# Optimization experiments

Hardware: AMD Instinct MI355X
Metric: run time of the kernel (lower is better)

Reference implementation:

```python
import jax, jax.numpy as jnp
import numpy as np

L = 256            # model length (match states)
Q = 2 * L + 3      # num_states = 2*length + 3
M = 1              # num_models
B = 256            # batch of sequences
T = 512            # sequence length (timesteps)
EPS = 1e-16


def setup_inputs() -> dict:
    key = jax.random.key(0)
    k1, k2, k3 = jax.random.split(key, 3)
    return {
        "emission_probs": jax.random.uniform(k1, (T, M, B, Q), dtype=jnp.float32),
        "log_A": jax.random.normal(k2, (M, Q, Q), dtype=jnp.float32),
        "init_logits": jax.random.normal(k3, (M, Q), dtype=jnp.float32),
    }


def reference(emission_probs, log_A, init_logits):
    # Dense transition matrix per model (row-stochastic), as in transitioner.make_log_A()
    A = jax.nn.softmax(log_A, axis=-1)                 # (M, Q, Q)
    init_dist = jax.nn.softmax(init_logits, axis=-1)   # (M, Q)

    def norm_step(E, R, ll):
        # One scaled-forward update: multiply emission, normalize, accumulate loglik.
        E = jnp.maximum(E, EPS)
        R = jnp.maximum(R, EPS)
        a = E * R                                      # (M, B, Q)
        S = jnp.sum(a, axis=-1, keepdims=True)         # (M, B, 1)
        ll = ll + jnp.log(S)
        a = a / S
        return a, ll

    # t = 0: init=True -> R is the initial distribution (no transition applied)
    R0 = jnp.broadcast_to(init_dist[:, None, :], (M, B, Q))
    fwd0, ll0 = norm_step(emission_probs[0], R0, jnp.zeros((M, B, 1), jnp.float32))
    out0 = jnp.concatenate([jnp.log(fwd0), ll0], axis=-1)  # (M, B, Q+1)

    def step(carry, E_t):
        fwd, ll = carry
        # transitioner(old_scaled_forward): dense transition matvec per model
        R = jnp.einsum('mbq,mqk->mbk', fwd, A)
        a, ll = norm_step(E_t, R, ll)
        return (a, ll), jnp.concatenate([jnp.log(a), ll], axis=-1)

    _, outs = jax.lax.scan(step, (fwd0, ll0), emission_probs[1:])
    outs = jnp.concatenate([out0[None], outs], axis=0)     # (T, M, B, Q+1)
    # RNN output layout: (M*B, T, Q+1)
    return jnp.transpose(outs, (1, 2, 0, 3)).reshape(M * B, T, Q + 1)
```

## Files before the change

### kernel.cpp

```cpp
#include <hip/hip_runtime.h>
#include <cstdint>

#define Qn   515
#define QP   520
#define QP2  528
#define Bn   256
#define Tn   512
#define OQ   516
#define EPSc 1e-16f
#define NSL  65
#define NT   5
#define KT   33
#define KTA  17
#define USTR 532
#define NGRP 32
#define NBLK 8

#define WS_AMAT 0
#define WS_INIT (544*520*4)
#define WS_UBUF (WS_INIT + 5120)
#define WS_PSUM (WS_UBUF + 2*NGRP*8*QP2*4)
#define WS_FLAG (WS_PSUM + 2*NGRP*8*8*4)
#define WS_TOTAL (WS_FLAG + NGRP*NBLK*64)

#define L_FRAG 0
#define L_UST  (NT*KT*64*8)
#define L_USL  (L_UST + 16*USTR*2)
#define L_SIG  (L_USL + 8*68*4)
#define LDS_TOTAL (L_SIG + 128)

typedef float f32x4 __attribute__((ext_vector_type(4)));
typedef short s16x4 __attribute__((ext_vector_type(4)));

__device__ __forceinline__ unsigned bfbits(float x) {
    unsigned u = __builtin_bit_cast(unsigned, x);
    unsigned r = u + 0x7FFFu + ((u >> 16) & 1u);
    return r >> 16;
}

__global__ void prep_A(const float* __restrict__ logA, float* __restrict__ AMAT) {
    __shared__ float red[4];
    __shared__ float srow[Qn];
    int row = blockIdx.x, tid = threadIdx.x;
    if (row >= Qn) {
        for (int c = tid; c < QP; c += 256) AMAT[(size_t)row*QP + c] = 0.f;
        return;
    }
    float mx = -1e30f;
    for (int c = tid; c < Qn; c += 256) { float x = logA[(size_t)row*Qn + c]; srow[c] = x; mx = fmaxf(mx, x); }
#pragma unroll
    for (int o = 32; o > 0; o >>= 1) mx = fmaxf(mx, __shfl_xor(mx, o));
    if ((tid & 63) == 0) red[tid >> 6] = mx;
    __syncthreads();
    mx = fmaxf(fmaxf(red[0], red[1]), fmaxf(red[2], red[3]));
    __syncthreads();
    float sm = 0.f;
    for (int c = tid; c < Qn; c += 256) sm += __expf(srow[c] - mx);
#pragma unroll
    for (int o = 32; o > 0; o >>= 1) sm += __shfl_xor(sm, o);
    if ((tid & 63) == 0) red[tid >> 6] = sm;
    __syncthreads();
    float inv = 1.f / (red[0] + red[1] + red[2] + red[3]);
    for (int c = tid; c < QP; c += 256)
        AMAT[(size_t)row*QP + c] = (c < Qn) ? __expf(srow[c] - mx) * inv : 0.f;
}

__global__ void prep_init(const float* __restrict__ il, float* __restrict__ INITD) {
    __shared__ float red[4];
    __shared__ float srow[Qn];
    int tid = threadIdx.x;
    float mx = -1e30f;
    for (int c = tid; c < Qn; c += 256) { float x = il[c]; srow[c] = x; mx = fmaxf(mx, x); }
#pragma unroll
    for (int o = 32; o > 0; o >>= 1) mx = fmaxf(mx, __shfl_xor(mx, o));
    if ((tid & 63) == 0) red[tid >> 6] = mx;
    __syncthreads();
    mx = fmaxf(fmaxf(red[0], red[1]), fmaxf(red[2], red[3]));
    __syncthreads();
    float sm = 0.f;
    for (int c = tid; c < Qn; c += 256) sm += __expf(srow[c] - mx);
#pragma unroll
    for (int o = 32; o > 0; o >>= 1) sm += __shfl_xor(sm, o);
    if ((tid & 63) == 0) red[tid >> 6] = sm;
    __syncthreads();
    float inv = 1.f / (red[0] + red[1] + red[2] + red[3]);
    for (int c = tid; c < QP; c += 256)
        INITD[c] = (c < Qn) ? __expf(srow[c] - mx) * inv : 0.f;
}

__global__ void __launch_bounds__(256, 1)
hmm_fwd(const float* __restrict__ E, const float* __restrict__ AMAT,
        const float* __restrict__ INITD, float* __restrict__ out,
        float* __restrict__ ubuf, float* __restrict__ psum,
        unsigned* __restrict__ flags)
{
    extern __shared__ char smem[];
    uint2*  frag   = (uint2*)(smem + L_FRAG);
    unsigned short* ustage = (unsigned short*)(smem + L_UST);
    float*  usl    = (float*)(smem + L_USL);
    float*  invs   = (float*)(smem + L_SIG);
    float*  lsig   = invs + 8;

    const int tid  = threadIdx.x;
    const int lane = tid & 63;
    const int wv   = tid >> 6;
    const int bid  = blockIdx.x;
    const int g    = bid & 31;
    const int j    = bid >> 5;
    const int b0   = g * 8;
    const int q0   = j * NSL;
    const int q0p  = j * 66;

    for (int f = tid; f < NT*KT*64; f += 256) {
        int tile = f >> 6, l = f & 63;
        int nt = tile / KT, kt = tile - nt*KT;
        int col = q0 + nt*16 + (l & 15);
        int kb  = kt*16 + ((l >> 4) << 2);
        float v[4];
#pragma unroll
        for (int i = 0; i < 4; ++i) {
            int pk_ = kb + i;
            int jr = pk_ / 66, rr = pk_ - jr*66;
            int qrow = (rr < 65) ? (jr*65 + rr) : -1;
            v[i] = (qrow >= 0 && col < QP) ? AMAT[(size_t)qrow*QP + col] : 0.f;
        }
        uint2 pk;
        pk.x = bfbits(v[0]) | (bfbits(v[1]) << 16);
        pk.y = bfbits(v[2]) | (bfbits(v[3]) << 16);
        frag[f] = pk;
    }
    for (int i = tid; i < 16*(USTR/2); i += 256) ((unsigned*)ustage)[i] = 0u;
    float llreg = 0.f;
    float ur0[9], ur1[9];
    __syncthreads();

    const int ntn = (wv == 0) ? 2 : 1;
    const int nts0 = wv;
    int eoff[2][4];
#pragma unroll
    for (int sl = 0; sl < 2; ++sl) {
#pragma unroll
        for (int r = 0; r < 4; ++r) {
            int nt  = sl ? 4 : nts0;
            int row = ((lane >> 4) << 2) + r;
            int col = nt*16 + (lane & 15);
            int q   = q0 + col;
            bool ok = (lane < 32) && (col < NSL) && (q < Qn) && (sl < ntn);
            eoff[sl][r] = ok ? ((b0 + row)*Qn + q) : -1;
        }
    }

    auto rowsum_store = [&](int wb, int snum) {
        int half = lane >> 5, c = lane & 31;
        int row = wv*2 + half;
        float v = usl[row*68 + c] + usl[row*68 + c + 32];
        if (c == 0) v += usl[row*68 + 64];
#pragma unroll
        for (int o = 16; o > 0; o >>= 1) v += __shfl_xor(v, o);
        if (c == 0)
            __hip_atomic_store(&psum[(((size_t)wb*NGRP + g)*8 + row)*8 + j], v,
                               __ATOMIC_RELAXED, __HIP_MEMORY_SCOPE_AGENT);
        float* ubr = ubuf + (((size_t)wb*NGRP + g)*8)*QP2 + q0p;
        for (int p = tid; p < 8*33; p += 256) {
            int rw = p/33, cl = p - rw*33;
            float a0 = usl[rw*68 + 2*cl];
            float a1 = (2*cl + 1 < NSL) ? usl[rw*68 + 2*cl + 1] : 0.f;
            uint64_t pk = (uint64_t)__builtin_bit_cast(unsigned, a0)
                        | ((uint64_t)__builtin_bit_cast(unsigned, a1) << 32);
            __hip_atomic_store((uint64_t*)(ubr + rw*QP2 + 2*cl), pk,
                               __ATOMIC_RELAXED, __HIP_MEMORY_SCOPE_AGENT);
        }
        __syncthreads();
        if (tid == 0)
            __hip_atomic_store(&flags[((unsigned)g*NBLK + j)*16], (unsigned)(snum + 1),
                               __ATOMIC_RELAXED, __HIP_MEMORY_SCOPE_AGENT);
    };

    auto spin_wait = [&](unsigned target) {
        if (tid < 8) {
            const unsigned* fp = flags + ((unsigned)g*NBLK + tid)*16;
            while (__hip_atomic_load(fp, __ATOMIC_RELAXED, __HIP_MEMORY_SCOPE_AGENT) < target)
                __builtin_amdgcn_s_sleep(1);
        }
        __syncthreads();
    };

    auto head_phase = [&](int rb, bool do_stage) {
        float ss = 0.f;
        if (tid < 8) {
            const float* pp = psum + (((size_t)rb*NGRP + g)*8 + tid)*8;
#pragma unroll
            for (int jj = 0; jj < 8; ++jj)
                ss += __hip_atomic_load(&pp[jj], __ATOMIC_RELAXED, __HIP_MEMORY_SCOPE_AGENT);
        }
        const float* ub = ubuf + (((size_t)rb*NGRP + g)*8)*QP2;
#pragma unroll
        for (int it = 0; it < 9; ++it) {
            int p = tid + it*256;
            bool ok = p < 8*264;
            int row = p / 264, kp = p - row*264;
            const uint64_t* ap = (const uint64_t*)(ub + (ok ? (row*QP2 + kp*2) : 0));
            uint64_t w = __hip_atomic_load(ap, __ATOMIC_RELAXED, __HIP_MEMORY_SCOPE_AGENT);
            ur0[it] = ok ? __builtin_bit_cast(float, (unsigned)(w & 0xffffffffu)) : 0.f;
            ur1[it] = ok ? __builtin_bit_cast(float, (unsigned)(w >> 32)) : 0.f;
        }
        if (tid < 8) {
            float ls = __logf(ss);
            invs[tid] = 1.f / ss;
            lsig[tid] = ls;
            llreg += ls;
        }
        __syncthreads();
        if (do_stage) {
#pragma unroll
            for (int it = 0; it < 9; ++it) {
                int p = tid + it*256;
                if (p < 8*264) {
                    int row = p / 264, kp = p - row*264;
                    float iv = invs[row];
                    ((unsigned*)ustage)[row*(USTR/2) + kp] =
                        bfbits(ur0[it]*iv) | (bfbits(ur1[it]*iv) << 16);
                }
            }
            __syncthreads();
        }
    };

    auto emit_outputs = [&](int tOut) {
        if (tid < 8 && j == 0)
            out[((size_t)(b0 + tid)*Tn + tOut)*OQ + Qn] = llreg;
#pragma unroll
        for (int it = 0; it < 9; ++it) {
            int p = tid + it*256;
            if (p < 8*264) {
                int row = p / 264, kp = p - row*264;
                int rr = kp*2 - q0p;
                if (rr >= 0 && rr < NSL) {
                    float ls = lsig[row];
                    int q = q0 + rr;
                    if (q < Qn)
                        out[((size_t)(b0+row)*Tn + tOut)*OQ + q]     = __logf(ur0[it]) - ls;
                    if (rr + 1 < NSL && q + 1 < Qn)
                        out[((size_t)(b0+row)*Tn + tOut)*OQ + q + 1] = __logf(ur1[it]) - ls;
                }
            }
        }
    };

    {
        for (int p = tid; p < 8*NSL; p += 256) {
            int row = p / NSL, col = p - row*NSL;
            int q = q0 + col;
            float uv = 0.f;
            if (q < Qn) {
                float e  = fmaxf(E[(size_t)(b0+row)*Qn + q], EPSc);
                float r0 = fmaxf(INITD[q], EPSc);
                uv = e * r0;
            }
            usl[row*68 + col] = uv;
        }
        __syncthreads();
        rowsum_store(0, 0);
    }

    for (int s = 1; s < Tn; ++s) {
        float ev[2][4];
        size_t ebase = (size_t)s * Bn * Qn;
#pragma unroll
        for (int sl = 0; sl < 2; ++sl)
#pragma unroll
            for (int r = 0; r < 4; ++r)
                ev[sl][r] = (eoff[sl][r] >= 0) ? E[ebase + eoff[sl][r]] : 0.f;

        spin_wait((unsigned)s);
        head_phase((s-1) & 1, true);

        f32x4 a0a = {0.f,0.f,0.f,0.f}, a0b = {0.f,0.f,0.f,0.f};
        f32x4 a1a = {0.f,0.f,0.f,0.f}, a1b = {0.f,0.f,0.f,0.f};
        {
            const unsigned short* urow = ustage + (lane & 15)*USTR + ((lane >> 4) << 2);
            const uint2* f0 = frag + (size_t)(nts0*KT)*64 + lane;
            const uint2* f1 = frag + (size_t)(4*KT)*64 + lane;
#pragma unroll 2
            for (int kt = 0; kt < KTA; ++kt) {
                s16x4 af = __builtin_bit_cast(s16x4, *(const uint2*)(urow + kt*16));
                a0a = __builtin_amdgcn_mfma_f32_16x16x16bf16_1k(af, __builtin_bit_cast(s16x4, f0[kt*64]), a0a, 0, 0, 0);
                if (ntn == 2)
                    a1a = __builtin_amdgcn_mfma_f32_16x16x16bf16_1k(af, __builtin_bit_cast(s16x4, f1[kt*64]), a1a, 0, 0, 0);
                int k2 = kt + KTA;
                if (k2 < KT) {
                    s16x4 af2 = __builtin_bit_cast(s16x4, *(const uint2*)(urow + k2*16));
                    a0b = __builtin_amdgcn_mfma_f32_16x16x16bf16_1k(af2, __builtin_bit_cast(s16x4, f0[k2*64]), a0b, 0, 0, 0);
                    if (ntn == 2)
                        a1b = __builtin_amdgcn_mfma_f32_16x16x16bf16_1k(af2, __builtin_bit_cast(s16x4, f1[k2*64]), a1b, 0, 0, 0);
                }
            }
        }
        if (lane < 32) {
#pragma unroll
            for (int r = 0; r < 4; ++r) {
                int row = ((lane >> 4) << 2) + r;
                {
                    int col = nts0*16 + (lane & 15);
                    if (col < NSL) {
                        float R = fmaxf(a0a[r] + a0b[r], EPSc);
                        int q = q0 + col;
                        usl[row*68 + col] = (q < Qn) ? fmaxf(ev[0][r], EPSc) * R : 0.f;
                    }
                }
                if (ntn == 2) {
                    int col = 64 + (lane & 15);
                    if (col < NSL) {
                        float R = fmaxf(a1a[r] + a1b[r], EPSc);
                        int q = q0 + col;
                        usl[row*68 + col] = (q < Qn) ? fmaxf(ev[1][r], EPSc) * R : 0.f;
                    }
                }
            }
        }
        __syncthreads();
        rowsum_store(s & 1, s);

        emit_outputs(s - 1);
    }

    spin_wait((unsigned)Tn);
    head_phase((Tn-1) & 1, false);
    emit_outputs(Tn - 1);
}

extern "C" void kernel_launch(void* const* d_in, const int* in_sizes, int n_in,
                              void* d_out, int out_size, void* d_ws, size_t ws_size,
                              hipStream_t stream) {
    (void)in_sizes; (void)n_in; (void)out_size;
    if (ws_size < (size_t)WS_TOTAL) return;

    const float* E    = (const float*)d_in[0];
    const float* logA = (const float*)d_in[1];
    const float* il   = (const float*)d_in[2];
    float* out = (float*)d_out;
    char*  ws  = (char*)d_ws;

    float*    AMAT  = (float*)(ws + WS_AMAT);
    float*    INITD = (float*)(ws + WS_INIT);
    float*    ubuf  = (float*)(ws + WS_UBUF);
    float*    psum  = (float*)(ws + WS_PSUM);
    unsigned* flags = (unsigned*)(ws + WS_FLAG);

    hipMemsetAsync(ws + WS_UBUF, 0, WS_TOTAL - WS_UBUF, stream);

    prep_A<<<544, 256, 0, stream>>>(logA, AMAT);
    prep_init<<<1, 256, 0, stream>>>(il, INITD);

    static_assert(LDS_TOTAL < 160*1024, "LDS budget");
    hipFuncSetAttribute(reinterpret_cast<const void*>(hmm_fwd),
                        hipFuncAttributeMaxDynamicSharedMemorySize, LDS_TOTAL);
    hmm_fwd<<<256, 256, LDS_TOTAL, stream>>>(E, AMAT, INITD, out, ubuf, psum, flags);
}
```

Measured before the change: 3.292 ms.

## Replace flag-based inter-block exchange with sequence-tagged values and workgroup-scope polling

Removes separate flags and partial-sum buffers. Each forward value is now packed with its timestep tag in a 64-bit word, and consumers poll the data words directly until all tags match. Each row's normalizer is computed redundantly from the full vector, so the per-block rowsum pass and a barrier go away. A startup probe checks whether blocks in a group can see each other through workgroup-scope (L1) loads with buffer_inv. If not, the kernel falls back to agent-scope dual stores. The transition matrix is also pre-packed to bf16 in the prep kernel. This relies on non-portable coherence assumptions and adds timing-dependent mode selection.

```diff
diff --git a/kernel.cpp b/kernel.cpp
--- a/kernel.cpp
+++ b/kernel.cpp
@@ -1,9 +1,12 @@
 #include <hip/hip_runtime.h>
 #include <cstdint>
 
+typedef unsigned long long u64;
+typedef float f32x4 __attribute__((ext_vector_type(4)));
+typedef short s16x4 __attribute__((ext_vector_type(4)));
+
 #define Qn   515
 #define QP   520
-#define QP2  528
 #define Bn   256
 #define Tn   512
 #define OQ   516
@@ -12,38 +15,42 @@
 #define NT   5
 #define KT   33
 #define KTA  17
+#define QPW  528
 #define USTR 532
 #define NGRP 32
 #define NBLK 8
 
-#define WS_AMAT 0
-#define WS_INIT (544*520*4)
-#define WS_UBUF (WS_INIT + 5120)
-#define WS_PSUM (WS_UBUF + 2*NGRP*8*QP2*4)
-#define WS_FLAG (WS_PSUM + 2*NGRP*8*8*4)
-#define WS_TOTAL (WS_FLAG + NGRP*NBLK*64)
+#define WS_AMATH 0
+#define WS_INIT  565760
+#define WS_FBUF  568320
+#define WS_SBUF  (WS_FBUF + 2162688)
+#define WS_CAN   (WS_SBUF + 2162688)
+#define WS_TOTAL (WS_CAN + 4096)
 
 #define L_FRAG 0
 #define L_UST  (NT*KT*64*8)
-#define L_USL  (L_UST + 16*USTR*2)
-#define L_SIG  (L_USL + 8*68*4)
-#define LDS_TOTAL (L_SIG + 128)
-
-typedef float f32x4 __attribute__((ext_vector_type(4)));
-typedef short s16x4 __attribute__((ext_vector_type(4)));
+#define LDS_TOTAL (L_UST + 16*USTR*2 + 16)
 
 __device__ __forceinline__ unsigned bfbits(float x) {
     unsigned u = __builtin_bit_cast(unsigned, x);
     unsigned r = u + 0x7FFFu + ((u >> 16) & 1u);
     return r >> 16;
 }
-
-__global__ void prep_A(const float* __restrict__ logA, float* __restrict__ AMAT) {
+__device__ __forceinline__ void l1_inv() {
+    asm volatile("buffer_inv" ::: "memory");
+}
+__device__ __forceinline__ void exch_store(u64* f, u64* s, u64 v, bool dual) {
+    __hip_atomic_store(f, v, __ATOMIC_RELAXED, __HIP_MEMORY_SCOPE_WORKGROUP);
+    if (dual)
+        __hip_atomic_store(s, v, __ATOMIC_RELAXED, __HIP_MEMORY_SCOPE_AGENT);
+}
+
+__global__ void prep_A(const float* __restrict__ logA, unsigned* __restrict__ AMATh) {
     __shared__ float red[4];
     __shared__ float srow[Qn];
     int row = blockIdx.x, tid = threadIdx.x;
     if (row >= Qn) {
-        for (int c = tid; c < QP; c += 256) AMAT[(size_t)row*QP + c] = 0.f;
+        for (int c = tid; c < 260; c += 256) AMATh[(size_t)row*260 + c] = 0u;
         return;
     }
     float mx = -1e30f;
@@ -61,8 +68,12 @@
     if ((tid & 63) == 0) red[tid >> 6] = sm;
     __syncthreads();
     float inv = 1.f / (red[0] + red[1] + red[2] + red[3]);
-    for (int c = tid; c < QP; c += 256)
-        AMAT[(size_t)row*QP + c] = (c < Qn) ? __expf(srow[c] - mx) * inv : 0.f;
+    for (int c2 = tid; c2 < 260; c2 += 256) {
+        int c = 2*c2;
+        float v0 = (c   < Qn) ? __expf(srow[c]   - mx) * inv : 0.f;
+        float v1 = (c+1 < Qn) ? __expf(srow[c+1] - mx) * inv : 0.f;
+        AMATh[(size_t)row*260 + c2] = bfbits(v0) | (bfbits(v1) << 16);
+    }
 }
 
 __global__ void prep_init(const float* __restrict__ il, float* __restrict__ INITD) {
@@ -84,22 +95,20 @@
     if ((tid & 63) == 0) red[tid >> 6] = sm;
     __syncthreads();
     float inv = 1.f / (red[0] + red[1] + red[2] + red[3]);
-    for (int c = tid; c < QP; c += 256)
+    for (int c = tid; c < 520; c += 256)
         INITD[c] = (c < Qn) ? __expf(srow[c] - mx) * inv : 0.f;
 }
 
 __global__ void __launch_bounds__(256, 1)
-hmm_fwd(const float* __restrict__ E, const float* __restrict__ AMAT,
+hmm_fwd(const float* __restrict__ E, const unsigned* __restrict__ AMATh,
         const float* __restrict__ INITD, float* __restrict__ out,
-        float* __restrict__ ubuf, float* __restrict__ psum,
-        unsigned* __restrict__ flags)
+        u64* __restrict__ fbuf, u64* __restrict__ sbuf,
+        unsigned* __restrict__ can)
 {
     extern __shared__ char smem[];
-    uint2*  frag   = (uint2*)(smem + L_FRAG);
+    uint2* frag = (uint2*)(smem + L_FRAG);
     unsigned short* ustage = (unsigned short*)(smem + L_UST);
-    float*  usl    = (float*)(smem + L_USL);
-    float*  invs   = (float*)(smem + L_SIG);
-    float*  lsig   = invs + 8;
+    __shared__ unsigned modeflag;
 
     const int tid  = threadIdx.x;
     const int lane = tid & 63;
@@ -111,28 +120,53 @@
     const int q0   = j * NSL;
     const int q0p  = j * 66;
 
+    if (tid == 0) {
+        unsigned slow = 0;
+        unsigned* myc = &can[(unsigned)g*NBLK + j];
+        for (int r = 0; r < 8 && !slow; ++r) {
+            __hip_atomic_store(myc, (unsigned)(r+1), __ATOMIC_RELAXED, __HIP_MEMORY_SCOPE_WORKGROUP);
+            long long limit = (r == 0) ? 8000000LL : 80000LL;
+            long long t0 = __builtin_readcyclecounter();
+            for (int p = 0; p < NBLK && !slow; ++p) {
+                if (p == j) continue;
+                while (true) {
+                    l1_inv();
+                    unsigned vv = __hip_atomic_load(&can[(unsigned)g*NBLK + p],
+                                                    __ATOMIC_RELAXED, __HIP_MEMORY_SCOPE_WORKGROUP);
+                    if (vv >= (unsigned)(r+1) && vv <= 8u) break;
+                    if (__builtin_readcyclecounter() - t0 > limit) { slow = 1; break; }
+                }
+            }
+        }
+        modeflag = slow;
+    }
+
     for (int f = tid; f < NT*KT*64; f += 256) {
         int tile = f >> 6, l = f & 63;
         int nt = tile / KT, kt = tile - nt*KT;
         int col = q0 + nt*16 + (l & 15);
         int kb  = kt*16 + ((l >> 4) << 2);
-        float v[4];
+        unsigned h[4];
 #pragma unroll
         for (int i = 0; i < 4; ++i) {
             int pk_ = kb + i;
             int jr = pk_ / 66, rr = pk_ - jr*66;
-            int qrow = (rr < 65) ? (jr*65 + rr) : -1;
-            v[i] = (qrow >= 0 && col < QP) ? AMAT[(size_t)qrow*QP + col] : 0.f;
+            unsigned hv = 0;
+            if (rr < 65 && col < QP) {
+                int qrow = jr*65 + rr;
+                unsigned w = AMATh[(size_t)qrow*260 + (col >> 1)];
+                hv = (col & 1) ? (w >> 16) : (w & 0xffffu);
+            }
+            h[i] = hv;
         }
         uint2 pk;
-        pk.x = bfbits(v[0]) | (bfbits(v[1]) << 16);
-        pk.y = bfbits(v[2]) | (bfbits(v[3]) << 16);
+        pk.x = h[0] | (h[1] << 16);
+        pk.y = h[2] | (h[3] << 16);
         frag[f] = pk;
     }
     for (int i = tid; i < 16*(USTR/2); i += 256) ((unsigned*)ustage)[i] = 0u;
-    float llreg = 0.f;
-    float ur0[9], ur1[9];
-    __syncthreads();
+    __syncthreads();
+    const bool slowmode = (modeflag != 0);
 
     const int ntn = (wv == 0) ? 2 : 1;
     const int nts0 = wv;
@@ -149,119 +183,81 @@
             eoff[sl][r] = ok ? ((b0 + row)*Qn + q) : -1;
         }
     }
-
-    auto rowsum_store = [&](int wb, int snum) {
-        int half = lane >> 5, c = lane & 31;
-        int row = wv*2 + half;
-        float v = usl[row*68 + c] + usl[row*68 + c + 32];
-        if (c == 0) v += usl[row*68 + 64];
-#pragma unroll
-        for (int o = 16; o > 0; o >>= 1) v += __shfl_xor(v, o);
-        if (c == 0)
-            __hip_atomic_store(&psum[(((size_t)wb*NGRP + g)*8 + row)*8 + j], v,
-                               __ATOMIC_RELAXED, __HIP_MEMORY_SCOPE_AGENT);
-        float* ubr = ubuf + (((size_t)wb*NGRP + g)*8)*QP2 + q0p;
-        for (int p = tid; p < 8*33; p += 256) {
-            int rw = p/33, cl = p - rw*33;
-            float a0 = usl[rw*68 + 2*cl];
-            float a1 = (2*cl + 1 < NSL) ? usl[rw*68 + 2*cl + 1] : 0.f;
-            uint64_t pk = (uint64_t)__builtin_bit_cast(unsigned, a0)
-                        | ((uint64_t)__builtin_bit_cast(unsigned, a1) << 32);
-            __hip_atomic_store((uint64_t*)(ubr + rw*QP2 + 2*cl), pk,
-                               __ATOMIC_RELAXED, __HIP_MEMORY_SCOPE_AGENT);
-        }
-        __syncthreads();
-        if (tid == 0)
-            __hip_atomic_store(&flags[((unsigned)g*NBLK + j)*16], (unsigned)(snum + 1),
-                               __ATOMIC_RELAXED, __HIP_MEMORY_SCOPE_AGENT);
+    const int rrow = tid >> 5;
+    const int t32  = tid & 31;
+
+    float llreg = 0.f;
+    float v[17];
+    float lsr = 0.f;
+
+    {
+        u64* fw = fbuf + ((size_t)0*NGRP + g)*8*QPW;
+        u64* sw = sbuf + ((size_t)0*NGRP + g)*8*QPW;
+        for (int p = tid; p < 8*66; p += 256) {
+            int row = p / 66, c = p - row*66;
+            int q = q0 + c;
+            float uv = 0.f;
+            if (c < 65 && q < Qn)
+                uv = fmaxf(E[(size_t)(b0+row)*Qn + q], EPSc) * fmaxf(INITD[q], EPSc);
+            u64 pk = (u64)__builtin_bit_cast(unsigned, uv) | ((u64)1u << 32);
+            exch_store(&fw[(size_t)row*QPW + q0p + c], &sw[(size_t)row*QPW + q0p + c], pk, slowmode);
+        }
+    }
+
+    auto poll_read = [&](int s) {
+        const size_t base = ((size_t)((s-1) & 1)*NGRP + g)*8*QPW + (size_t)rrow*QPW;
+        const u64* fb = fbuf + base;
+        const u64* sb = sbuf + base;
+        unsigned want = (unsigned)s;
+        u64 w[17];
+        unsigned pend = (t32 < 16) ? 0x1FFFFu : 0xFFFFu;
+        int iter = 0;
+        while (true) {
+            l1_inv();
+            bool sp = slowmode && ((iter & 3) == 3);
+#pragma unroll
+            for (int k = 0; k < 17; ++k) {
+                if (pend & (1u << k)) {
+                    int pc = t32 + 32*k;
+                    w[k] = sp ? __hip_atomic_load(&sb[pc], __ATOMIC_RELAXED, __HIP_MEMORY_SCOPE_AGENT)
+                              : __hip_atomic_load(&fb[pc], __ATOMIC_RELAXED, __HIP_MEMORY_SCOPE_WORKGROUP);
+                }
+            }
+#pragma unroll
+            for (int k = 0; k < 17; ++k)
+                if ((pend & (1u << k)) && (unsigned)(w[k] >> 32) == want) pend &= ~(1u << k);
+            if (pend == 0) break;
+            if (slowmode) __builtin_amdgcn_s_sleep(1);
+            ++iter;
+        }
+        float sum = 0.f;
+#pragma unroll
+        for (int k = 0; k < 17; ++k) {
+            int pc = t32 + 32*k;
+            v[k] = (pc < QPW) ? __builtin_bit_cast(float, (unsigned)(w[k] & 0xffffffffu)) : 0.f;
+            sum += v[k];
+        }
+#pragma unroll
+        for (int o = 1; o < 32; o <<= 1) sum += __shfl_xor(sum, o);
+        lsr = __logf(sum);
+        llreg += lsr;
+        return 1.f / sum;
     };
 
-    auto spin_wait = [&](unsigned target) {
-        if (tid < 8) {
-            const unsigned* fp = flags + ((unsigned)g*NBLK + tid)*16;
-            while (__hip_atomic_load(fp, __ATOMIC_RELAXED, __HIP_MEMORY_SCOPE_AGENT) < target)
-                __builtin_amdgcn_s_sleep(1);
-        }
-        __syncthreads();
+    auto emit_outputs = [&](int tOut) {
+        if (j == 0 && t32 == 0)
+            out[((size_t)(b0 + rrow)*Tn + tOut)*OQ + Qn] = llreg;
+#pragma unroll
+        for (int k = 0; k < 17; ++k) {
+            int pc = t32 + 32*k;
+            int c = pc - q0p;
+            if (pc < QPW && c >= 0 && c < 65) {
+                int q = q0 + c;
+                if (q < Qn)
+                    out[((size_t)(b0 + rrow)*Tn + tOut)*OQ + q] = __logf(v[k]) - lsr;
+            }
+        }
     };
-
-    auto head_phase = [&](int rb, bool do_stage) {
-        float ss = 0.f;
-        if (tid < 8) {
-            const float* pp = psum + (((size_t)rb*NGRP + g)*8 + tid)*8;
-#pragma unroll
-            for (int jj = 0; jj < 8; ++jj)
-                ss += __hip_atomic_load(&pp[jj], __ATOMIC_RELAXED, __HIP_MEMORY_SCOPE_AGENT);
-        }
-        const float* ub = ubuf + (((size_t)rb*NGRP + g)*8)*QP2;
-#pragma unroll
-        for (int it = 0; it < 9; ++it) {
-            int p = tid + it*256;
-            bool ok = p < 8*264;
-            int row = p / 264, kp = p - row*264;
-            const uint64_t* ap = (const uint64_t*)(ub + (ok ? (row*QP2 + kp*2) : 0));
-            uint64_t w = __hip_atomic_load(ap, __ATOMIC_RELAXED, __HIP_MEMORY_SCOPE_AGENT);
-            ur0[it] = ok ? __builtin_bit_cast(float, (unsigned)(w & 0xffffffffu)) : 0.f;
-            ur1[it] = ok ? __builtin_bit_cast(float, (unsigned)(w >> 32)) : 0.f;
-        }
-        if (tid < 8) {
-            float ls = __logf(ss);
-            invs[tid] = 1.f / ss;
-            lsig[tid] = ls;
-            llreg += ls;
-        }
-        __syncthreads();
-        if (do_stage) {
-#pragma unroll
-            for (int it = 0; it < 9; ++it) {
-                int p = tid + it*256;
-                if (p < 8*264) {
-                    int row = p / 264, kp = p - row*264;
-                    float iv = invs[row];
-                    ((unsigned*)ustage)[row*(USTR/2) + kp] =
-                        bfbits(ur0[it]*iv) | (bfbits(ur1[it]*iv) << 16);
-                }
-            }
-            __syncthreads();
-        }
-    };
-
-    auto emit_outputs = [&](int tOut) {
-        if (tid < 8 && j == 0)
-            out[((size_t)(b0 + tid)*Tn + tOut)*OQ + Qn] = llreg;
-#pragma unroll
-        for (int it = 0; it < 9; ++it) {
-            int p = tid + it*256;
-            if (p < 8*264) {
-                int row = p / 264, kp = p - row*264;
-                int rr = kp*2 - q0p;
-                if (rr >= 0 && rr < NSL) {
-                    float ls = lsig[row];
-                    int q = q0 + rr;
-                    if (q < Qn)
-                        out[((size_t)(b0+row)*Tn + tOut)*OQ + q]     = __logf(ur0[it]) - ls;
-                    if (rr + 1 < NSL && q + 1 < Qn)
-                        out[((size_t)(b0+row)*Tn + tOut)*OQ + q + 1] = __logf(ur1[it]) - ls;
-                }
-            }
-        }
-    };
-
-    {
-        for (int p = tid; p < 8*NSL; p += 256) {
-            int row = p / NSL, col = p - row*NSL;
-            int q = q0 + col;
-            float uv = 0.f;
-            if (q < Qn) {
-                float e  = fmaxf(E[(size_t)(b0+row)*Qn + q], EPSc);
-                float r0 = fmaxf(INITD[q], EPSc);
-                uv = e * r0;
-            }
-            usl[row*68 + col] = uv;
-        }
-        __syncthreads();
-        rowsum_store(0, 0);
-    }
 
     for (int s = 1; s < Tn; ++s) {
         float ev[2][4];
@@ -272,8 +268,16 @@
             for (int r = 0; r < 4; ++r)
                 ev[sl][r] = (eoff[sl][r] >= 0) ? E[ebase + eoff[sl][r]] : 0.f;
 
-        spin_wait((unsigned)s);
-        head_phase((s-1) & 1, true);
+        float inv = poll_read(s);
+
+        __syncthreads();
+#pragma unroll
+        for (int k = 0; k < 17; ++k) {
+            int pc = t32 + 32*k;
+            if (pc < QPW)
+                ustage[rrow*USTR + pc] = (unsigned short)bfbits(v[k] * inv);
+        }
+        __syncthreads();
 
         f32x4 a0a = {0.f,0.f,0.f,0.f}, a0b = {0.f,0.f,0.f,0.f};
         f32x4 a1a = {0.f,0.f,0.f,0.f}, a1b = {0.f,0.f,0.f,0.f};
@@ -296,36 +300,46 @@
                 }
             }
         }
-        if (lane < 32) {
-#pragma unroll
-            for (int r = 0; r < 4; ++r) {
-                int row = ((lane >> 4) << 2) + r;
-                {
-                    int col = nts0*16 + (lane & 15);
-                    if (col < NSL) {
+        {
+            unsigned seqv = (unsigned)(s + 1);
+            size_t wbase = ((size_t)(s & 1)*NGRP + g)*8*QPW;
+            u64* fw = fbuf + wbase;
+            u64* sw = sbuf + wbase;
+            if (lane < 32) {
+#pragma unroll
+                for (int r = 0; r < 4; ++r) {
+                    int row = ((lane >> 4) << 2) + r;
+                    {
+                        int col = nts0*16 + (lane & 15);
                         float R = fmaxf(a0a[r] + a0b[r], EPSc);
                         int q = q0 + col;
-                        usl[row*68 + col] = (q < Qn) ? fmaxf(ev[0][r], EPSc) * R : 0.f;
+                        float uv = (q < Qn) ? fmaxf(ev[0][r], EPSc) * R : 0.f;
+                        u64 pk = (u64)__builtin_bit_cast(unsigned, uv) | ((u64)seqv << 32);
+                        size_t off = (size_t)row*QPW + q0p + col;
+                        exch_store(&fw[off], &sw[off], pk, slowmode);
+                    }
+                    if (ntn == 2 && (lane & 15) == 0) {
+                        int col = 64;
+                        float R = fmaxf(a1a[r] + a1b[r], EPSc);
+                        int q = q0 + col;
+                        float uv = (q < Qn) ? fmaxf(ev[1][r], EPSc) * R : 0.f;
+                        u64 pk = (u64)__builtin_bit_cast(unsigned, uv) | ((u64)seqv << 32);
+                        size_t off = (size_t)row*QPW + q0p + col;
+                        exch_store(&fw[off], &sw[off], pk, slowmode);
                     }
                 }
-                if (ntn == 2) {
-                    int col = 64 + (lane & 15);
-                    if (col < NSL) {
-                        float R = fmaxf(a1a[r] + a1b[r], EPSc);
-                        int q = q0 + col;
-                        usl[row*68 + col] = (q < Qn) ? fmaxf(ev[1][r], EPSc) * R : 0.f;
-                    }
-                }
-            }
-        }
-        __syncthreads();
-        rowsum_store(s & 1, s);
-
+            }
+            if (wv == 1 && lane >= 32 && lane < 40) {
+                int row = lane - 32;
+                u64 pk = ((u64)seqv << 32);
+                size_t off = (size_t)row*QPW + q0p + 65;
+                exch_store(&fw[off], &sw[off], pk, slowmode);
+            }
+        }
         emit_outputs(s - 1);
     }
 
-    spin_wait((unsigned)Tn);
-    head_phase((Tn-1) & 1, false);
+    poll_read(Tn);
     emit_outputs(Tn - 1);
 }
 
@@ -341,19 +355,19 @@
     float* out = (float*)d_out;
     char*  ws  = (char*)d_ws;
 
-    float*    AMAT  = (float*)(ws + WS_AMAT);
+    unsigned* AMATh = (unsigned*)(ws + WS_AMATH);
     float*    INITD = (float*)(ws + WS_INIT);
-    float*    ubuf  = (float*)(ws + WS_UBUF);
-    float*    psum  = (float*)(ws + WS_PSUM);
-    unsigned* flags = (unsigned*)(ws + WS_FLAG);
-
-    hipMemsetAsync(ws + WS_UBUF, 0, WS_TOTAL - WS_UBUF, stream);
-
-    prep_A<<<544, 256, 0, stream>>>(logA, AMAT);
+    u64*      fbuf  = (u64*)(ws + WS_FBUF);
+    u64*      sbuf  = (u64*)(ws + WS_SBUF);
+    unsigned* can   = (unsigned*)(ws + WS_CAN);
+
+    hipMemsetAsync(ws + WS_CAN, 0, 4096, stream);
+
+    prep_A<<<544, 256, 0, stream>>>(logA, AMATh);
     prep_init<<<1, 256, 0, stream>>>(il, INITD);
 
     static_assert(LDS_TOTAL < 160*1024, "LDS budget");
     hipFuncSetAttribute(reinterpret_cast<const void*>(hmm_fwd),
                         hipFuncAttributeMaxDynamicSharedMemorySize, LDS_TOTAL);
-    hmm_fwd<<<256, 256, LDS_TOTAL, stream>>>(E, AMAT, INITD, out, ubuf, psum, flags);
-}
+    hmm_fwd<<<256, 256, LDS_TOTAL, stream>>>(E, AMATh, INITD, out, fbuf, sbuf, can);
+}
```

Result: slower. 6.803 ms (+106.7%).
